# Kernel optimization log

Hardware: AMD Instinct MI355X
Metric: run time of the kernel (lower is better)

The kernel has to match this reference:

```python
import jax, jax.numpy as jnp
import numpy as np

B, T, DIM = 2, 2048, 2048
N_HEAD, N_GROUP = 16, 4
KV_HEAD = N_HEAD // N_GROUP
HEAD_DIM = DIM // N_HEAD


def setup_inputs() -> dict:
    key = jax.random.key(0)
    ks = jax.random.split(key, 7)
    x = jax.random.normal(ks[0], (B, T, DIM), dtype=jnp.float32)
    # rotary tables: last dim = head_dim // 2 (interleaved real/imag pairs)
    pos = jnp.arange(T, dtype=jnp.float32)[:, None]
    inv_freq = 1.0 / (10000.0 ** (jnp.arange(0, HEAD_DIM, 2, dtype=jnp.float32) / HEAD_DIM))
    angles = pos * inv_freq[None, :]  # [T, HEAD_DIM//2]
    freqs_cos = jnp.cos(angles)
    freqs_sin = jnp.sin(angles)
    scale = 0.02
    wq = jax.random.normal(ks[1], (DIM, N_HEAD * HEAD_DIM), dtype=jnp.float32) * scale
    wk = jax.random.normal(ks[2], (DIM, KV_HEAD * HEAD_DIM), dtype=jnp.float32) * scale
    wv = jax.random.normal(ks[3], (DIM, KV_HEAD * HEAD_DIM), dtype=jnp.float32) * scale
    wo = jax.random.normal(ks[4], (N_HEAD * HEAD_DIM, DIM), dtype=jnp.float32) * scale
    return {"x": x, "freqs_cos": freqs_cos, "freqs_sin": freqs_sin,
            "wq": wq, "wk": wk, "wv": wv, "wo": wo}


def _apply_rope(t, cos, sin):
    # t: [B, T, H, D]; interleaved pairs (..., -1, 2) as in torch reference
    tr = t.reshape(*t.shape[:-1], -1, 2)
    r, i = tr[..., 0], tr[..., 1]
    c = cos[None, :, None, :]  # [1, T, 1, D//2]
    s = sin[None, :, None, :]
    out = jnp.stack([r * c - i * s, r * s + i * c], axis=-1)
    return out.reshape(t.shape)


def reference(x, freqs_cos, freqs_sin, wq, wk, wv, wo):
    Bx, Tx, C = x.shape
    xq = (x @ wq).reshape(Bx, Tx, N_HEAD, HEAD_DIM)
    xk = (x @ wk).reshape(Bx, Tx, KV_HEAD, HEAD_DIM)
    xv = (x @ wv).reshape(Bx, Tx, KV_HEAD, HEAD_DIM)
    xq = _apply_rope(xq, freqs_cos, freqs_sin)
    xk = _apply_rope(xk, freqs_cos, freqs_sin)
    # repeat_kv: each kv head repeated n_group times consecutively
    xk = jnp.repeat(xk, N_GROUP, axis=2)  # [B, T, N_HEAD, D]
    xv = jnp.repeat(xv, N_GROUP, axis=2)
    scale = HEAD_DIM ** -0.5
    att = jnp.einsum('bqhd,bkhd->bhqk', xq, xk) * scale
    causal = jnp.tril(jnp.ones((Tx, Tx), dtype=bool))
    att = jnp.where(causal[None, None], att, -jnp.inf)
    att = jax.nn.softmax(att, axis=-1)
    out = jnp.einsum('bhqk,bkhd->bqhd', att, xv).reshape(Bx, Tx, N_HEAD * HEAD_DIM)
    return out @ wo
```

## Files before the change

kernel.cpp:

```cpp
#include <hip/hip_runtime.h>

#define TB 2
#define TT 2048
#define TDIM 2048
#define NHEADS 16
#define KVHEADS 4
#define HD 128

typedef unsigned short u16;
typedef unsigned int u32;
typedef __attribute__((ext_vector_type(8))) short short8;
typedef __attribute__((ext_vector_type(4))) float float4_t;

__device__ __forceinline__ float b2f(u16 u) {
    union { u32 i; float f; } v; v.i = ((u32)u) << 16; return v.f;
}
__device__ __forceinline__ u16 f2b(float f) {
    union { float f; u32 i; } v; v.f = f;
    u32 r = (v.i + 0x7FFFu + ((v.i >> 16) & 1u)) >> 16;
    return (u16)r;
}
__device__ __forceinline__ u32 fbits(float f) {
    union { float f; u32 i; } v; v.f = f; return v.i;
}

__device__ __forceinline__ void gl_lds16(const void* g, void* l) {
    __builtin_amdgcn_global_load_lds((const __attribute__((address_space(1))) void*)g,
                                     (__attribute__((address_space(3))) void*)l, 16, 0, 0);
}

template <bool F32OUT, bool ROPE>
__global__ __launch_bounds__(256, 3)
void gemm_bt(const u16* __restrict__ A, const u16* __restrict__ BT,
             void* __restrict__ Cv, int M, int N, int K,
             const float* __restrict__ fc, const float* __restrict__ fs) {
    __shared__ __align__(16) u16 As[128 * 64];
    __shared__ __align__(16) u16 Bs[128 * 64];
    const int tid  = threadIdx.x;
    const int wave = tid >> 6, lane = tid & 63;
    const int quad = lane >> 4, l16 = lane & 15;
    const int wm = wave >> 1, wn = wave & 1;
    const int row0 = blockIdx.y * 128, col0 = blockIdx.x * 128;

    float4_t acc[4][4];
#pragma unroll
    for (int i = 0; i < 4; i++)
#pragma unroll
        for (int j = 0; j < 4; j++) acc[i][j] = (float4_t){0.f, 0.f, 0.f, 0.f};

    for (int kk = 0; kk < K; kk += 64) {
        __syncthreads();
#pragma unroll
        for (int i = 0; i < 4; i++) {
            int n = i * 256 + wave * 64 + lane;
            int r = n >> 3, c = (n & 7) ^ (r & 7);
            gl_lds16(A  + (size_t)(row0 + r) * K + kk + c * 8, &As[(i * 256 + wave * 64) * 8]);
            gl_lds16(BT + (size_t)(col0 + r) * K + kk + c * 8, &Bs[(i * 256 + wave * 64) * 8]);
        }
        __syncthreads();
#pragma unroll
        for (int ks = 0; ks < 2; ks++) {
            short8 af[4], bf[4];
#pragma unroll
            for (int mt = 0; mt < 4; mt++) {
                int m = wm * 64 + mt * 16 + l16;
                af[mt] = *(const short8*)&As[(m * 8 + ((ks * 4 + quad) ^ (l16 & 7))) * 8];
            }
#pragma unroll
            for (int nt = 0; nt < 4; nt++) {
                int n = wn * 64 + nt * 16 + l16;
                bf[nt] = *(const short8*)&Bs[(n * 8 + ((ks * 4 + quad) ^ (l16 & 7))) * 8];
            }
#pragma unroll
            for (int mt = 0; mt < 4; mt++)
#pragma unroll
                for (int nt = 0; nt < 4; nt++)
                    acc[mt][nt] = __builtin_amdgcn_mfma_f32_16x16x32_bf16(
                        af[mt], bf[nt], acc[mt][nt], 0, 0, 0);
        }
    }
    const bool do_rope = ROPE && (col0 < 2560);
#pragma unroll
    for (int mt = 0; mt < 4; mt++)
#pragma unroll
        for (int nt = 0; nt < 4; nt++)
#pragma unroll
            for (int r = 0; r < 4; r++) {
                int row = row0 + wm * 64 + mt * 16 + quad * 4 + r;
                int col = col0 + wn * 64 + nt * 16 + l16;
                float v = acc[mt][nt][r];
                if (ROPE && do_rope) {
                    float other = __shfl_xor(v, 1, 64);
                    int t = row & (TT - 1);
                    int i0 = (col & (HD - 1)) >> 1;
                    float c = fc[t * 64 + i0], s = fs[t * 64 + i0];
                    v = (col & 1) ? fmaf(v, c, other * s) : fmaf(v, c, -other * s);
                }
                if (F32OUT)
                    ((float*)Cv)[(size_t)row * N + col] = v;
                else
                    ((u16*)Cv)[(size_t)row * N + col] = f2b(v);
            }
}

__global__ void prep(const float* __restrict__ x, u16* __restrict__ xb,
                     const float* __restrict__ wq, const float* __restrict__ wk,
                     const float* __restrict__ wv, const float* __restrict__ wo,
                     u16* __restrict__ WT, u16* __restrict__ woT) {
    const int bid = blockIdx.x;
    if (bid < 8192) {
        size_t i = ((size_t)bid * 256 + threadIdx.x) * 4;
        float4 v = *(const float4*)(x + i);
        ushort4 o;
        o.x = f2b(v.x); o.y = f2b(v.y); o.z = f2b(v.z); o.w = f2b(v.w);
        *(ushort4*)(xb + i) = o;
        return;
    }
    const int rem = bid - 8192;
    const int bx = rem % 160;
    const int by = rem / 160;
    const float* in; u16* out; int cols, cx;
    if (bx < 64)      { in = wq; out = WT;                         cols = 2048; cx = bx; }
    else if (bx < 80) { in = wk; out = WT + (size_t)2048 * 2048;   cols = 512;  cx = bx - 64; }
    else if (bx < 96) { in = wv; out = WT + (size_t)2560 * 2048;   cols = 512;  cx = bx - 80; }
    else              { in = wo; out = woT;                        cols = 2048; cx = bx - 96; }
    const int rows = 2048;
    __shared__ u16 tile[32][33];
    int c0 = cx * 32, r0 = by * 32;
    int tx = threadIdx.x & 31, ty = threadIdx.x >> 5;
#pragma unroll
    for (int i = 0; i < 4; i++)
        tile[ty + i * 8][tx] = f2b(in[(size_t)(r0 + ty + i * 8) * cols + c0 + tx]);
    __syncthreads();
#pragma unroll
    for (int i = 0; i < 4; i++)
        out[(size_t)(c0 + ty + i * 8) * rows + r0 + tx] = tile[tx][ty + i * 8];
}

__global__ void transpose_v(const u16* __restrict__ QKV, u16* __restrict__ Vt) {
    int z = blockIdx.z, b = z >> 2, kv = z & 3;
    const u16* in = QKV + (size_t)b * TT * 3072 + 2560 + kv * HD;
    u16* out = Vt + (size_t)z * HD * TT;
    __shared__ u16 tile[32][33];
    int t0 = blockIdx.x * 32, d0 = blockIdx.y * 32;
    int tx = threadIdx.x & 31, ty = threadIdx.x >> 5;
#pragma unroll
    for (int i = 0; i < 4; i++)
        tile[ty + i * 8][tx] = in[(size_t)(t0 + ty + i * 8) * 3072 + d0 + tx];
    __syncthreads();
#pragma unroll
    for (int i = 0; i < 4; i++)
        out[(size_t)(d0 + ty + i * 8) * TT + t0 + tx] = tile[tx][ty + i * 8];
}

#define PSTR 72
__global__ __launch_bounds__(256, 2)
void attn(const u16* __restrict__ QKV, const u16* __restrict__ Vt,
          u16* __restrict__ O) {
    const int x  = blockIdx.x;
    const int y  = blockIdx.y;
    const int b  = y >> 3;
    const int hp = y & 7;
    const int kvh = hp >> 1;
    const int hb  = kvh * 4 + (hp & 1) * 2;
    const int qb  = b ? (31 - x) : x;
    const int tid = threadIdx.x, w = tid >> 6, lane = tid & 63;
    const int quad = lane >> 4, l16 = lane & 15;

    __shared__ __align__(16) u16 Ks[2][64 * 128];
    __shared__ __align__(16) u16 Vs[128 * 64];
    __shared__ __align__(16) u16 Ps[8][16 * PSTR];

    const u16* Kbase = QKV + (size_t)b * TT * 3072 + 2048 + kvh * HD;
    const u16* Vbase = Vt + (size_t)(b * 4 + kvh) * HD * TT;
    const float Cl = 0.12753102474f;

    auto stageK = [&](int kt, int bb) {
#pragma unroll
        for (int i = 0; i < 4; i++) {
            int n = i * 256 + w * 64 + lane;
            int r = n >> 4, c = (n & 15) ^ (r & 15);
            gl_lds16(Kbase + (size_t)(kt * 64 + r) * 3072 + c * 8,
                     &Ks[bb][(i * 256 + w * 64) * 8]);
        }
    };
    auto stageV = [&](int kt) {
#pragma unroll
        for (int i = 0; i < 4; i++) {
            int n = i * 256 + w * 64 + lane;
            int d = n >> 3, c = (n & 7) ^ (d & 7);
            gl_lds16(Vbase + (size_t)d * TT + kt * 64 + c * 8,
                     &Vs[(i * 256 + w * 64) * 8]);
        }
    };

    stageK(0, 0);

    short8 qf[2][4];
#pragma unroll
    for (int hd = 0; hd < 2; hd++) {
        const u16* Qrow = QKV + ((size_t)b * TT + qb * 64 + w * 16 + l16) * 3072
                          + (hb + hd) * HD;
#pragma unroll
        for (int ks = 0; ks < 4; ks++)
            qf[hd][ks] = *(const short8*)(Qrow + ks * 32 + quad * 8);
    }

    float4_t o[2][8];
#pragma unroll
    for (int hd = 0; hd < 2; hd++)
#pragma unroll
        for (int i = 0; i < 8; i++) o[hd][i] = (float4_t){0.f, 0.f, 0.f, 0.f};
    float mi[2] = {-1e30f, -1e30f}, li[2] = {0.f, 0.f};
    const int qg = qb * 64 + w * 16 + l16;

    for (int kt = 0; kt <= qb; kt++) {
        const int cur = kt & 1;
        __syncthreads();
        stageV(kt);

        float4_t st[2][4];
#pragma unroll
        for (int hd = 0; hd < 2; hd++)
#pragma unroll
            for (int nt = 0; nt < 4; nt++) st[hd][nt] = (float4_t){0.f, 0.f, 0.f, 0.f};
#pragma unroll
        for (int ks = 0; ks < 4; ks++) {
            short8 af[4];
#pragma unroll
            for (int nt = 0; nt < 4; nt++)
                af[nt] = *(const short8*)&Ks[cur][((nt * 16 + l16) * 16 +
                                                  ((ks * 4 + quad) ^ l16)) * 8];
            __builtin_amdgcn_s_setprio(1);
#pragma unroll
            for (int nt = 0; nt < 4; nt++) {
                st[0][nt] = __builtin_amdgcn_mfma_f32_16x16x32_bf16(
                    af[nt], qf[0][ks], st[0][nt], 0, 0, 0);
                st[1][nt] = __builtin_amdgcn_mfma_f32_16x16x32_bf16(
                    af[nt], qf[1][ks], st[1][nt], 0, 0, 0);
            }
            __builtin_amdgcn_s_setprio(0);
        }

        const bool diag = (kt == qb);
#pragma unroll
        for (int hd = 0; hd < 2; hd++) {
            if (diag) {
#pragma unroll
                for (int nt = 0; nt < 4; nt++)
#pragma unroll
                    for (int r = 0; r < 4; r++) {
                        int key = kt * 64 + nt * 16 + quad * 4 + r;
                        if (key > qg) st[hd][nt][r] = -3e38f;
                    }
            }
            float pm = -3e38f;
#pragma unroll
            for (int nt = 0; nt < 4; nt++)
#pragma unroll
                for (int r = 0; r < 4; r++) pm = fmaxf(pm, st[hd][nt][r]);
            pm = fmaxf(pm, __shfl_xor(pm, 16, 64));
            pm = fmaxf(pm, __shfl_xor(pm, 32, 64));
            const bool need = !__all(pm - mi[hd] <= 62.7f);
            float alpha_v = 1.f;
            if (need) {
                float mnew = fmaxf(mi[hd], pm);
                alpha_v = __builtin_amdgcn_exp2f((mi[hd] - mnew) * Cl);
                mi[hd] = mnew;
            }
            const float mC = mi[hd] * Cl;
            float rs = 0.f;
#pragma unroll
            for (int nt = 0; nt < 4; nt++)
#pragma unroll
                for (int r = 0; r < 4; r++) {
                    float e = __builtin_amdgcn_exp2f(fmaf(st[hd][nt][r], Cl, -mC));
                    st[hd][nt][r] = e;
                    rs += e;
                }
            rs += __shfl_xor(rs, 16, 64);
            rs += __shfl_xor(rs, 32, 64);
            li[hd] = li[hd] * alpha_v + rs;

#pragma unroll
            for (int nt = 0; nt < 4; nt++) {
                uint2 pk;
                pk.x = __builtin_amdgcn_perm(fbits(st[hd][nt][1]), fbits(st[hd][nt][0]), 0x07060302u);
                pk.y = __builtin_amdgcn_perm(fbits(st[hd][nt][3]), fbits(st[hd][nt][2]), 0x07060302u);
                *(uint2*)&Ps[w * 2 + hd][l16 * PSTR + nt * 16 + quad * 4] = pk;
            }
            if (need) {
                float a_o[4];
#pragma unroll
                for (int r = 0; r < 4; r++) a_o[r] = __shfl(alpha_v, quad * 4 + r, 64);
#pragma unroll
                for (int n2 = 0; n2 < 8; n2++)
#pragma unroll
                    for (int r = 0; r < 4; r++) o[hd][n2][r] *= a_o[r];
            }
        }

        __syncthreads();
        if (kt < qb) stageK(kt + 1, cur ^ 1);

#pragma unroll
        for (int ks2 = 0; ks2 < 2; ks2++) {
            short8 apA = *(const short8*)&Ps[w * 2 + 0][l16 * PSTR + ks2 * 32 + quad * 8];
            short8 apB = *(const short8*)&Ps[w * 2 + 1][l16 * PSTR + ks2 * 32 + quad * 8];
            __builtin_amdgcn_s_setprio(1);
#pragma unroll
            for (int n2 = 0; n2 < 8; n2++) {
                short8 bv = *(const short8*)&Vs[((n2 * 16 + l16) * 8 +
                                                ((ks2 * 4 + quad) ^ (l16 & 7))) * 8];
                o[0][n2] = __builtin_amdgcn_mfma_f32_16x16x32_bf16(apA, bv, o[0][n2], 0, 0, 0);
                o[1][n2] = __builtin_amdgcn_mfma_f32_16x16x32_bf16(apB, bv, o[1][n2], 0, 0, 0);
            }
            __builtin_amdgcn_s_setprio(0);
        }
    }

#pragma unroll
    for (int hd = 0; hd < 2; hd++) {
        float linv[4];
#pragma unroll
        for (int r = 0; r < 4; r++) linv[r] = 1.0f / __shfl(li[hd], quad * 4 + r, 64);
        u16* Ob2 = O + ((size_t)b * TT + qb * 64 + w * 16) * TDIM + (hb + hd) * HD;
#pragma unroll
        for (int n2 = 0; n2 < 8; n2++)
#pragma unroll
            for (int r = 0; r < 4; r++)
                Ob2[(size_t)(quad * 4 + r) * TDIM + n2 * 16 + l16] =
                    f2b(o[hd][n2][r] * linv[r]);
    }
}

extern "C" void kernel_launch(void* const* d_in, const int* in_sizes, int n_in,
                              void* d_out, int out_size, void* d_ws, size_t ws_size,
                              hipStream_t stream) {
    const float* x  = (const float*)d_in[0];
    const float* fc = (const float*)d_in[1];
    const float* fs = (const float*)d_in[2];
    const float* wq = (const float*)d_in[3];
    const float* wk = (const float*)d_in[4];
    const float* wv = (const float*)d_in[5];
    const float* wo = (const float*)d_in[6];
    float* out = (float*)d_out;

    char* ws = (char*)d_ws;
    size_t off = 0;
    auto alloc = [&](size_t bytes) -> void* {
        void* p = ws + off;
        off += (bytes + 255) & ~(size_t)255;
        return p;
    };
    u16* xb  = (u16*)alloc((size_t)4096 * 2048 * 2);
    u16* WT  = (u16*)alloc((size_t)3072 * 2048 * 2);
    u16* woT = (u16*)alloc((size_t)2048 * 2048 * 2);
    u16* QKV = (u16*)alloc((size_t)4096 * 3072 * 2);
    u16* Vtb = (u16*)alloc((size_t)4096 * 512 * 2);
    u16* Ob  = (u16*)alloc((size_t)4096 * 2048 * 2);

    dim3 blk(256);
    prep<<<dim3(8192 + 160 * 64), blk, 0, stream>>>(x, xb, wq, wk, wv, wo, WT, woT);
    gemm_bt<false, true><<<dim3(24, 32), blk, 0, stream>>>(
        xb, WT, QKV, 4096, 3072, 2048, fc, fs);
    transpose_v<<<dim3(64, 4, 8), blk, 0, stream>>>(QKV, Vtb);
    attn<<<dim3(32, 16), blk, 0, stream>>>(QKV, Vtb, Ob);
    gemm_bt<true, false><<<dim3(16, 32), blk, 0, stream>>>(
        Ob, woT, out, 4096, 2048, 2048, nullptr, nullptr);
}
```

Before: 311.5 us.

## Process one head per block with paired causal q-blocks for load balance

The attention kernel stops computing two query heads per block that share a staged K/V tile. Each block now handles a single head and loops over two query blocks (p and 31-p), so every block does the same amount of causal work. The grid changes from 32x16 to 16x32. K/V tiles are no longer shared across two heads, which doubles K/V staging traffic per unit of MFMA work. Fewer live accumulators lower register pressure, and the longer per-block runtime evens out the workload.

```diff
diff --git a/kernel.cpp b/kernel.cpp
--- a/kernel.cpp
+++ b/kernel.cpp
@@ -157,19 +157,17 @@
 __global__ __launch_bounds__(256, 2)
 void attn(const u16* __restrict__ QKV, const u16* __restrict__ Vt,
           u16* __restrict__ O) {
-    const int x  = blockIdx.x;
+    const int p  = blockIdx.x;
     const int y  = blockIdx.y;
-    const int b  = y >> 3;
-    const int hp = y & 7;
-    const int kvh = hp >> 1;
-    const int hb  = kvh * 4 + (hp & 1) * 2;
-    const int qb  = b ? (31 - x) : x;
+    const int b  = y >> 4;
+    const int h  = y & 15;
+    const int kvh = h >> 2;
     const int tid = threadIdx.x, w = tid >> 6, lane = tid & 63;
     const int quad = lane >> 4, l16 = lane & 15;
 
     __shared__ __align__(16) u16 Ks[2][64 * 128];
     __shared__ __align__(16) u16 Vs[128 * 64];
-    __shared__ __align__(16) u16 Ps[8][16 * PSTR];
+    __shared__ __align__(16) u16 Ps[4][16 * PSTR];
 
     const u16* Kbase = QKV + (size_t)b * TT * 3072 + 2048 + kvh * HD;
     const u16* Vbase = Vt + (size_t)(b * 4 + kvh) * HD * TT;
@@ -194,100 +192,91 @@
         }
     };
 
-    stageK(0, 0);
-
-    short8 qf[2][4];
-#pragma unroll
-    for (int hd = 0; hd < 2; hd++) {
-        const u16* Qrow = QKV + ((size_t)b * TT + qb * 64 + w * 16 + l16) * 3072
-                          + (hb + hd) * HD;
-#pragma unroll
-        for (int ks = 0; ks < 4; ks++)
-            qf[hd][ks] = *(const short8*)(Qrow + ks * 32 + quad * 8);
-    }
-
-    float4_t o[2][8];
-#pragma unroll
-    for (int hd = 0; hd < 2; hd++)
-#pragma unroll
-        for (int i = 0; i < 8; i++) o[hd][i] = (float4_t){0.f, 0.f, 0.f, 0.f};
-    float mi[2] = {-1e30f, -1e30f}, li[2] = {0.f, 0.f};
-    const int qg = qb * 64 + w * 16 + l16;
-
-    for (int kt = 0; kt <= qb; kt++) {
-        const int cur = kt & 1;
-        __syncthreads();
-        stageV(kt);
-
-        float4_t st[2][4];
-#pragma unroll
-        for (int hd = 0; hd < 2; hd++)
-#pragma unroll
-            for (int nt = 0; nt < 4; nt++) st[hd][nt] = (float4_t){0.f, 0.f, 0.f, 0.f};
-#pragma unroll
-        for (int ks = 0; ks < 4; ks++) {
-            short8 af[4];
-#pragma unroll
-            for (int nt = 0; nt < 4; nt++)
-                af[nt] = *(const short8*)&Ks[cur][((nt * 16 + l16) * 16 +
-                                                  ((ks * 4 + quad) ^ l16)) * 8];
-            __builtin_amdgcn_s_setprio(1);
-#pragma unroll
-            for (int nt = 0; nt < 4; nt++) {
-                st[0][nt] = __builtin_amdgcn_mfma_f32_16x16x32_bf16(
-                    af[nt], qf[0][ks], st[0][nt], 0, 0, 0);
-                st[1][nt] = __builtin_amdgcn_mfma_f32_16x16x32_bf16(
-                    af[nt], qf[1][ks], st[1][nt], 0, 0, 0);
-            }
-            __builtin_amdgcn_s_setprio(0);
-        }
-
-        const bool diag = (kt == qb);
-#pragma unroll
-        for (int hd = 0; hd < 2; hd++) {
-            if (diag) {
+    for (int pass = 0; pass < 2; pass++) {
+        const int qb = pass ? (31 - p) : p;
+        stageK(0, 0);
+
+        short8 qf[4];
+        {
+            const u16* Qrow = QKV + ((size_t)b * TT + qb * 64 + w * 16 + l16) * 3072
+                              + h * HD;
+#pragma unroll
+            for (int ks = 0; ks < 4; ks++)
+                qf[ks] = *(const short8*)(Qrow + ks * 32 + quad * 8);
+        }
+
+        float4_t o[8];
+#pragma unroll
+        for (int i = 0; i < 8; i++) o[i] = (float4_t){0.f, 0.f, 0.f, 0.f};
+        float mi = -1e30f, li = 0.f;
+        const int qg = qb * 64 + w * 16 + l16;
+
+        for (int kt = 0; kt <= qb; kt++) {
+            const int cur = kt & 1;
+            __syncthreads();
+            stageV(kt);
+
+            float4_t st[4];
+#pragma unroll
+            for (int nt = 0; nt < 4; nt++) st[nt] = (float4_t){0.f, 0.f, 0.f, 0.f};
+#pragma unroll
+            for (int ks = 0; ks < 4; ks++) {
+                short8 af[4];
+#pragma unroll
+                for (int nt = 0; nt < 4; nt++)
+                    af[nt] = *(const short8*)&Ks[cur][((nt * 16 + l16) * 16 +
+                                                      ((ks * 4 + quad) ^ l16)) * 8];
+                __builtin_amdgcn_s_setprio(1);
+#pragma unroll
+                for (int nt = 0; nt < 4; nt++)
+                    st[nt] = __builtin_amdgcn_mfma_f32_16x16x32_bf16(
+                        af[nt], qf[ks], st[nt], 0, 0, 0);
+                __builtin_amdgcn_s_setprio(0);
+            }
+
+            if (kt == qb) {
 #pragma unroll
                 for (int nt = 0; nt < 4; nt++)
 #pragma unroll
                     for (int r = 0; r < 4; r++) {
                         int key = kt * 64 + nt * 16 + quad * 4 + r;
-                        if (key > qg) st[hd][nt][r] = -3e38f;
+                        if (key > qg) st[nt][r] = -3e38f;
                     }
             }
             float pm = -3e38f;
 #pragma unroll
             for (int nt = 0; nt < 4; nt++)
 #pragma unroll
-                for (int r = 0; r < 4; r++) pm = fmaxf(pm, st[hd][nt][r]);
+                for (int r = 0; r < 4; r++) pm = fmaxf(pm, st[nt][r]);
             pm = fmaxf(pm, __shfl_xor(pm, 16, 64));
             pm = fmaxf(pm, __shfl_xor(pm, 32, 64));
-            const bool need = !__all(pm - mi[hd] <= 62.7f);
+            const bool need = !__all(pm - mi <= 62.7f);
             float alpha_v = 1.f;
             if (need) {
-                float mnew = fmaxf(mi[hd], pm);
-                alpha_v = __builtin_amdgcn_exp2f((mi[hd] - mnew) * Cl);
-                mi[hd] = mnew;
-            }
-            const float mC = mi[hd] * Cl;
+                float mnew = fmaxf(mi, pm);
+                alpha_v = __builtin_amdgcn_exp2f((mi - mnew) * Cl);
+                mi = mnew;
+            }
+            const float mC = mi * Cl;
             float rs = 0.f;
 #pragma unroll
             for (int nt = 0; nt < 4; nt++)
 #pragma unroll
                 for (int r = 0; r < 4; r++) {
-                    float e = __builtin_amdgcn_exp2f(fmaf(st[hd][nt][r], Cl, -mC));
-                    st[hd][nt][r] = e;
+                    float e = __builtin_amdgcn_exp2f(fmaf(st[nt][r], Cl, -mC));
+                    st[nt][r] = e;
                     rs += e;
                 }
             rs += __shfl_xor(rs, 16, 64);
             rs += __shfl_xor(rs, 32, 64);
-            li[hd] = li[hd] * alpha_v + rs;
+            li = li * alpha_v + rs;
 
 #pragma unroll
             for (int nt = 0; nt < 4; nt++) {
                 uint2 pk;
-                pk.x = __builtin_amdgcn_perm(fbits(st[hd][nt][1]), fbits(st[hd][nt][0]), 0x07060302u);
-                pk.y = __builtin_amdgcn_perm(fbits(st[hd][nt][3]), fbits(st[hd][nt][2]), 0x07060302u);
-                *(uint2*)&Ps[w * 2 + hd][l16 * PSTR + nt * 16 + quad * 4] = pk;
+                pk.x = __builtin_amdgcn_perm(fbits(st[nt][1]), fbits(st[nt][0]), 0x07060302u);
+                pk.y = __builtin_amdgcn_perm(fbits(st[nt][3]), fbits(st[nt][2]), 0x07060302u);
+                *(uint2*)&Ps[w][l16 * PSTR + nt * 16 + quad * 4] = pk;
             }
             if (need) {
                 float a_o[4];
@@ -296,41 +285,36 @@
 #pragma unroll
                 for (int n2 = 0; n2 < 8; n2++)
 #pragma unroll
-                    for (int r = 0; r < 4; r++) o[hd][n2][r] *= a_o[r];
-            }
-        }
-
-        __syncthreads();
-        if (kt < qb) stageK(kt + 1, cur ^ 1);
-
-#pragma unroll
-        for (int ks2 = 0; ks2 < 2; ks2++) {
-            short8 apA = *(const short8*)&Ps[w * 2 + 0][l16 * PSTR + ks2 * 32 + quad * 8];
-            short8 apB = *(const short8*)&Ps[w * 2 + 1][l16 * PSTR + ks2 * 32 + quad * 8];
-            __builtin_amdgcn_s_setprio(1);
-#pragma unroll
-            for (int n2 = 0; n2 < 8; n2++) {
-                short8 bv = *(const short8*)&Vs[((n2 * 16 + l16) * 8 +
-                                                ((ks2 * 4 + quad) ^ (l16 & 7))) * 8];
-                o[0][n2] = __builtin_amdgcn_mfma_f32_16x16x32_bf16(apA, bv, o[0][n2], 0, 0, 0);
-                o[1][n2] = __builtin_amdgcn_mfma_f32_16x16x32_bf16(apB, bv, o[1][n2], 0, 0, 0);
-            }
-            __builtin_amdgcn_s_setprio(0);
-        }
-    }
-
-#pragma unroll
-    for (int hd = 0; hd < 2; hd++) {
+                    for (int r = 0; r < 4; r++) o[n2][r] *= a_o[r];
+            }
+
+            __syncthreads();
+            if (kt < qb) stageK(kt + 1, cur ^ 1);
+
+#pragma unroll
+            for (int ks2 = 0; ks2 < 2; ks2++) {
+                short8 ap = *(const short8*)&Ps[w][l16 * PSTR + ks2 * 32 + quad * 8];
+                __builtin_amdgcn_s_setprio(1);
+#pragma unroll
+                for (int n2 = 0; n2 < 8; n2++) {
+                    short8 bv = *(const short8*)&Vs[((n2 * 16 + l16) * 8 +
+                                                    ((ks2 * 4 + quad) ^ (l16 & 7))) * 8];
+                    o[n2] = __builtin_amdgcn_mfma_f32_16x16x32_bf16(ap, bv, o[n2], 0, 0, 0);
+                }
+                __builtin_amdgcn_s_setprio(0);
+            }
+        }
+
         float linv[4];
 #pragma unroll
-        for (int r = 0; r < 4; r++) linv[r] = 1.0f / __shfl(li[hd], quad * 4 + r, 64);
-        u16* Ob2 = O + ((size_t)b * TT + qb * 64 + w * 16) * TDIM + (hb + hd) * HD;
+        for (int r = 0; r < 4; r++) linv[r] = 1.0f / __shfl(li, quad * 4 + r, 64);
+        u16* Ob2 = O + ((size_t)b * TT + qb * 64 + w * 16) * TDIM + h * HD;
 #pragma unroll
         for (int n2 = 0; n2 < 8; n2++)
 #pragma unroll
             for (int r = 0; r < 4; r++)
                 Ob2[(size_t)(quad * 4 + r) * TDIM + n2 * 16 + l16] =
-                    f2b(o[hd][n2][r] * linv[r]);
+                    f2b(o[n2][r] * linv[r]);
     }
 }
 
@@ -365,7 +349,7 @@
     gemm_bt<false, true><<<dim3(24, 32), blk, 0, stream>>>(
         xb, WT, QKV, 4096, 3072, 2048, fc, fs);
     transpose_v<<<dim3(64, 4, 8), blk, 0, stream>>>(QKV, Vtb);
-    attn<<<dim3(32, 16), blk, 0, stream>>>(QKV, Vtb, Ob);
+    attn<<<dim3(16, 32), blk, 0, stream>>>(QKV, Vtb, Ob);
     gemm_bt<true, false><<<dim3(16, 32), blk, 0, stream>>>(
         Ob, woT, out, 4096, 2048, 2048, nullptr, nullptr);
 }
```

New measurement: 305.1 us. 2.1% less time.
